# Kernel optimization log

Hardware: AMD Instinct MI355X
Metric: run time of the kernel (lower is better)

Reference implementation:

```python
import jax, jax.numpy as jnp
import numpy as np

B, T, C, H = 4, 2048, 1024, 16
D = C // H  # head dim = 64

def setup_inputs() -> dict:
    key = jax.random.key(0)
    k1, k2, k3 = jax.random.split(key, 3)
    x = jax.random.normal(k1, (B, T, C), dtype=jnp.float32)
    # torch Linear weight [out,in]; store transposed for x @ W
    W_attn = jax.random.normal(k2, (C, 3 * C), dtype=jnp.float32) * (1.0 / np.sqrt(C))
    W_proj = jax.random.normal(k3, (C, C), dtype=jnp.float32) * (1.0 / np.sqrt(C))
    return {"x": x, "W_attn": W_attn, "W_proj": W_proj}

def reference(x, W_attn, W_proj):
    qkv = x @ W_attn                          # [B,T,3C]
    q, k, v = jnp.split(qkv, 3, axis=-1)
    # [B,T,C] -> [B,H,T,D]
    def heads(t):
        return t.reshape(B, T, H, D).transpose(0, 2, 1, 3)
    q, k, v = heads(q), heads(k), heads(v)
    att = jnp.einsum('bhqd,bhkd->bhqk', q, k) * (1.0 / np.sqrt(D))  # [B,H,T,T]
    causal = jnp.tril(jnp.ones((T, T), dtype=bool))
    att = jnp.where(causal[None, None, :, :], att, -jnp.inf)
    att = jax.nn.softmax(att, axis=-1)
    y = jnp.einsum('bhqk,bhkd->bhqd', att, v)  # [B,H,T,D]
    y = y.transpose(0, 2, 1, 3).reshape(B, T, C)
    return y @ W_proj
```

## Files before the change

### kernel.cpp

```cpp
#include <hip/hip_runtime.h>
#include <hip/hip_bf16.h>

#define BB 4
#define TT 2048
#define CC 1024
#define HH 16
#define DD 64
#define MM (BB*TT)

typedef unsigned short u16;
typedef __bf16 bf16x8 __attribute__((ext_vector_type(8)));
typedef __bf16 bf16x4v __attribute__((ext_vector_type(4)));
typedef u16 u16x8 __attribute__((ext_vector_type(8)));
typedef u16 u16x4 __attribute__((ext_vector_type(4)));
typedef float f32x4 __attribute__((ext_vector_type(4)));

__device__ __forceinline__ u16 f2bf(float f) {
  union { float f; unsigned u; } v; v.f = f;
  unsigned u = v.u;
  return (u16)((u + 0x7fffu + ((u >> 16) & 1u)) >> 16);
}
__device__ __forceinline__ float bf2f(u16 s) {
  union { unsigned u; float f; } v; v.u = ((unsigned)s) << 16; return v.f;
}
__device__ __forceinline__ bf16x8 ld_bf16x8(const u16* p) {
  return *reinterpret_cast<const bf16x8*>(p);
}
__device__ __forceinline__ f32x4 zero4() {
  f32x4 z; z[0] = 0.f; z[1] = 0.f; z[2] = 0.f; z[3] = 0.f; return z;
}

__device__ __forceinline__ void gld_lds16(const u16* g, u16* l) {
  __builtin_amdgcn_global_load_lds(
      (const __attribute__((address_space(1))) void*)g,
      (__attribute__((address_space(3))) void*)l, 16, 0, 0);
}
__device__ __forceinline__ void wait_vm0() { __builtin_amdgcn_s_waitcnt(0x0F70); }
__device__ __forceinline__ void wait_vm2() { __builtin_amdgcn_s_waitcnt(0x0F72); }
__device__ __forceinline__ void wait_vm4() { __builtin_amdgcn_s_waitcnt(0x0F74); }

__device__ __forceinline__ float lane_pull(float x, int srclane) {
  int r = __builtin_amdgcn_ds_bpermute(srclane << 2, __builtin_bit_cast(int, x));
  return __builtin_bit_cast(float, r);
}

#define NC4B ((MM * CC / 4) / 256)
__global__ void k_prep(const float* __restrict__ x, u16* __restrict__ xb,
                       const float* __restrict__ Wa, u16* __restrict__ Wab,
                       const float* __restrict__ Wp, u16* __restrict__ Wpb) {
  __shared__ float tile[32][33];
  const int bx = blockIdx.x;
  if (bx < NC4B) {
    int i = bx * 256 + threadIdx.x;
    const float4 v = reinterpret_cast<const float4*>(x)[i];
    u16x4 r; r.x = f2bf(v.x); r.y = f2bf(v.y); r.z = f2bf(v.z); r.w = f2bf(v.w);
    reinterpret_cast<u16x4*>(xb)[i] = r;
    return;
  }
  const float* W; u16* Wt; int K, N, b2;
  if (bx < NC4B + 3072) { W = Wa; Wt = Wab; K = CC; N = 3 * CC; b2 = bx - NC4B; }
  else                  { W = Wp; Wt = Wpb; K = CC; N = CC;     b2 = bx - NC4B - 3072; }
  const int nblk = N / 32;
  const int nb = (b2 % nblk) * 32, kb = (b2 / nblk) * 32;
  const int tx = threadIdx.x & 31, ty = threadIdx.x >> 5;
  #pragma unroll
  for (int i = ty; i < 32; i += 8)
    tile[i][tx] = W[(size_t)(kb + i) * N + nb + tx];
  __syncthreads();
  #pragma unroll
  for (int i = ty; i < 32; i += 8)
    Wt[(size_t)(nb + i) * K + kb + tx] = f2bf(tile[tx][i]);
}

template<int EPI>
__global__ __launch_bounds__(256, 3)
void k_gemm_bt(const u16* __restrict__ A, const u16* __restrict__ Bt,
               float* __restrict__ outF, u16* __restrict__ qb, u16* __restrict__ kb,
               u16* __restrict__ vt, int N, int K)
{
  __shared__ u16 As[128 * 64];
  __shared__ u16 Bs[128 * 64];
  const int tid  = threadIdx.x;
  const int lane = tid & 63, w = tid >> 6;
  const int l16  = lane & 15, quad = lane >> 4;
  const int wr = w >> 1, wc = w & 1;
  const int m0 = blockIdx.y * 128, n0 = blockIdx.x * 128;
  const int lr8 = lane >> 3, lc8 = lane & 7;

  f32x4 acc[4][4];
  #pragma unroll
  for (int i = 0; i < 4; ++i)
    #pragma unroll
    for (int j = 0; j < 4; ++j) acc[i][j] = zero4();

  for (int k0 = 0; k0 < K; k0 += 64) {
    __syncthreads();
    #pragma unroll
    for (int p = 0; p < 4; ++p) {
      const int row = w * 32 + p * 8 + lr8;
      const int cs  = lc8 ^ (row & 7);
      gld_lds16(A  + (size_t)(m0 + row) * K + k0 + cs * 8, &As[(w * 32 + p * 8) * 64]);
      gld_lds16(Bt + (size_t)(n0 + row) * K + k0 + cs * 8, &Bs[(w * 32 + p * 8) * 64]);
    }
    wait_vm0();
    __syncthreads();
    #pragma unroll
    for (int s = 0; s < 2; ++s) {
      bf16x8 af[4], bfr[4];
      #pragma unroll
      for (int i = 0; i < 4; ++i) {
        int mrow = wr * 64 + i * 16 + l16;
        af[i]  = ld_bf16x8(&As[mrow * 64 + ((s * 4 + quad) ^ (l16 & 7)) * 8]);
        int nrow = wc * 64 + i * 16 + l16;
        bfr[i] = ld_bf16x8(&Bs[nrow * 64 + ((s * 4 + quad) ^ (l16 & 7)) * 8]);
      }
      #pragma unroll
      for (int i = 0; i < 4; ++i)
        #pragma unroll
        for (int j = 0; j < 4; ++j)
          acc[i][j] = __builtin_amdgcn_mfma_f32_16x16x32_bf16(af[i], bfr[j], acc[i][j], 0, 0, 0);
    }
  }

  #pragma unroll
  for (int i = 0; i < 4; ++i) {
    #pragma unroll
    for (int j = 0; j < 4; ++j) {
      const int n = n0 + wc * 64 + j * 16 + l16;
      const int mb = m0 + wr * 64 + i * 16 + quad * 4;
      if (EPI == 0) {
        #pragma unroll
        for (int r = 0; r < 4; ++r)
          outF[(size_t)(mb + r) * N + n] = acc[i][j][r];
      } else {
        const int b = mb >> 11, tb = mb & 2047;
        if (n < CC) {
          const int h = n >> 6, d = n & 63;
          #pragma unroll
          for (int r = 0; r < 4; ++r)
            qb[(((size_t)(b * HH + h) * TT + tb + r) << 6) + d] = f2bf(acc[i][j][r]);
        } else if (n < 2 * CC) {
          const int n2 = n - CC; const int h = n2 >> 6, d = n2 & 63;
          #pragma unroll
          for (int r = 0; r < 4; ++r)
            kb[(((size_t)(b * HH + h) * TT + tb + r) << 6) + d] = f2bf(acc[i][j][r]);
        } else {
          const int n2 = n - 2 * CC; const int h = n2 >> 6, d = n2 & 63;
          u16x4 cv;
          #pragma unroll
          for (int r = 0; r < 4; ++r) cv[r] = f2bf(acc[i][j][r]);
          *reinterpret_cast<u16x4*>(
              vt + ((size_t)(b * HH + h) * DD + d) * TT + tb) = cv;
        }
      }
    }
  }
}

__device__ __forceinline__ void stage_half256(const u16* __restrict__ G, u16* lbase,
                                              int grow0, int kk, int lr8, int lc8) {
  const int cs = (lc8 ^ lr8) << 3;
  gld_lds16(G + (size_t)(grow0 + lr8) * CC + kk + cs, lbase);
  gld_lds16(G + (size_t)(grow0 + 8 + lr8) * CC + kk + cs, lbase + 8 * 64);
}

__global__ __launch_bounds__(512, 2)
void k_gemm256(const u16* __restrict__ A, const u16* __restrict__ Bt,
               u16* __restrict__ qb, u16* __restrict__ kbuf, u16* __restrict__ vt)
{
  __shared__ u16 As[2][256 * 64];
  __shared__ u16 Bs[2][256 * 64];
  const int tid  = threadIdx.x;
  const int lane = tid & 63, w = tid >> 6;
  const int l16  = lane & 15, quad = lane >> 4;
  const int lr8  = lane >> 3, lc8 = lane & 7;
  const int wm = w >> 2, wn = w & 3;

  const int lin = blockIdx.x;
  const int nl  = (lin & 7) * 48 + (lin >> 3);
  const int mt  = nl / 12, nt_ = nl % 12;
  const int m0 = mt * 256, n0 = nt_ * 256;

  f32x4 acc[4][4][2];
  #pragma unroll
  for (int q = 0; q < 4; ++q)
    #pragma unroll
    for (int i = 0; i < 4; ++i)
      #pragma unroll
      for (int j = 0; j < 2; ++j) acc[q][i][j] = zero4();

  stage_half256(A,  &As[0][(0 * 128 + w * 16) * 64], m0 +       w * 16, 0, lr8, lc8);
  stage_half256(Bt, &Bs[0][(0 * 128 + w * 16) * 64], n0 +       w * 16, 0, lr8, lc8);
  stage_half256(Bt, &Bs[0][(1 * 128 + w * 16) * 64], n0 + 128 + w * 16, 0, lr8, lc8);
  stage_half256(A,  &As[0][(1 * 128 + w * 16) * 64], m0 + 128 + w * 16, 0, lr8, lc8);
  wait_vm4();
  __builtin_amdgcn_s_barrier();

  for (int t = 0; t < 16; ++t) {
    const int bb = t & 1;
    const bool notlast = (t < 15);
    const int kk = (t + 1) << 6;
    #pragma unroll
    for (int q = 0; q < 4; ++q) {
      const int qm = (q >> 1);
      const int qn = (q == 1 || q == 2);
      bf16x8 af[2][4], bfr[2][2];
      #pragma unroll
      for (int s = 0; s < 2; ++s) {
        const int cs = ((s * 4 + quad) ^ (l16 & 7)) << 3;
        #pragma unroll
        for (int i = 0; i < 4; ++i)
          af[s][i] = ld_bf16x8(&As[bb][(qm * 128 + wm * 64 + i * 16 + l16) * 64 + cs]);
        #pragma unroll
        for (int j = 0; j < 2; ++j)
          bfr[s][j] = ld_bf16x8(&Bs[bb][(qn * 128 + wn * 32 + j * 16 + l16) * 64 + cs]);
      }
      if (notlast) {
        if (q == 0)
          stage_half256(A,  &As[bb ^ 1][(0 * 128 + w * 16) * 64], m0 +       w * 16, kk, lr8, lc8);
        else if (q == 1)
          stage_half256(Bt, &Bs[bb ^ 1][(0 * 128 + w * 16) * 64], n0 +       w * 16, kk, lr8, lc8);
        else if (q == 2)
          stage_half256(Bt, &Bs[bb ^ 1][(1 * 128 + w * 16) * 64], n0 + 128 + w * 16, kk, lr8, lc8);
        else
          stage_half256(A,  &As[bb ^ 1][(1 * 128 + w * 16) * 64], m0 + 128 + w * 16, kk, lr8, lc8);
      }
      __builtin_amdgcn_s_setprio(1);
      #pragma unroll
      for (int s = 0; s < 2; ++s)
        #pragma unroll
        for (int i = 0; i < 4; ++i)
          #pragma unroll
          for (int j = 0; j < 2; ++j)
            acc[q][i][j] = __builtin_amdgcn_mfma_f32_16x16x32_bf16(
                af[s][i], bfr[s][j], acc[q][i][j], 0, 0, 0);
      __builtin_amdgcn_s_setprio(0);
      if (notlast)       wait_vm4();
      else if (q == 0)   wait_vm2();
      else if (q == 1)   wait_vm0();
      __builtin_amdgcn_s_barrier();
    }
  }

  #pragma unroll
  for (int q = 0; q < 4; ++q) {
    const int qm = (q >> 1);
    const int qn = (q == 1 || q == 2);
    #pragma unroll
    for (int i = 0; i < 4; ++i) {
      #pragma unroll
      for (int j = 0; j < 2; ++j) {
        const int n  = n0 + qn * 128 + wn * 32 + j * 16 + l16;
        const int mb = m0 + qm * 128 + wm * 64 + i * 16 + quad * 4;
        const int b = mb >> 11, tb = mb & 2047;
        if (n < CC) {
          const int h = n >> 6, d = n & 63;
          #pragma unroll
          for (int r = 0; r < 4; ++r)
            qb[(((size_t)(b * HH + h) * TT + tb + r) << 6) + d] = f2bf(acc[q][i][j][r]);
        } else if (n < 2 * CC) {
          const int n2 = n - CC; const int h = n2 >> 6, d = n2 & 63;
          #pragma unroll
          for (int r = 0; r < 4; ++r)
            kbuf[(((size_t)(b * HH + h) * TT + tb + r) << 6) + d] = f2bf(acc[q][i][j][r]);
        } else {
          const int n2 = n - 2 * CC; const int h = n2 >> 6, d = n2 & 63;
          u16x4 cv;
          #pragma unroll
          for (int r = 0; r < 4; ++r) cv[r] = f2bf(acc[q][i][j][r]);
          *reinterpret_cast<u16x4*>(
              vt + ((size_t)(b * HH + h) * DD + d) * TT + tb) = cv;
        }
      }
    }
  }
}

__global__ __launch_bounds__(256, 3)
void k_attn(const u16* __restrict__ qb, const u16* __restrict__ kb,
            const u16* __restrict__ vt, u16* __restrict__ y)
{
  __shared__ u16 Ks[128 * 64];
  __shared__ u16 Vs[64 * 128];
  __shared__ u16 QP[8 * 1024];
  const int tid  = threadIdx.x;
  const int lane = tid & 63, w = tid >> 6;
  const int l16  = lane & 15, quad = lane >> 4;
  const int lr8 = lane >> 3, lc8 = lane & 7;

  const int bx = blockIdx.x;
  const int qt = 15 - (bx >> 6);
  const int bh = bx & 63;
  const int h  = bh & 15, b = bh >> 4;

  const u16* qptr = qb + ((size_t)bh * TT + qt * 128) * DD;
  const u16* kptr = kb + (size_t)bh * TT * DD;
  const u16* vptr = vt + (size_t)bh * DD * TT;

  const float qscale = 0.125f * 1.44269504088896340736f;
  #pragma unroll
  for (int p = 0; p < 4; ++p) {
    const int r = w * 32 + p * 8 + lr8;
    u16x8 v = *reinterpret_cast<const u16x8*>(qptr + (size_t)r * DD + lc8 * 8);
    u16x8 o;
    #pragma unroll
    for (int e = 0; e < 8; ++e) o[e] = f2bf(bf2f(v[e]) * qscale);
    *reinterpret_cast<u16x8*>(&Ks[r * 64 + (lc8 ^ lr8) * 8]) = o;
  }
  __syncthreads();
  bf16x8 qf0[2], qf1[2];
  #pragma unroll
  for (int s = 0; s < 2; ++s) {
    qf0[s] = ld_bf16x8(&Ks[(w * 16 + l16) * 64 + ((s * 4 + quad) ^ (l16 & 7)) * 8]);
    qf1[s] = ld_bf16x8(&Ks[(64 + w * 16 + l16) * 64 + ((s * 4 + quad) ^ (l16 & 7)) * 8]);
  }

  float rsum0 = 0.f, rsum1 = 0.f;
  f32x4 O0[4], O1[4];
  #pragma unroll
  for (int j = 0; j < 4; ++j) { O0[j] = zero4(); O1[j] = zero4(); }

  const int nkt = qt + 1;
  for (int kt = 0; kt < nkt; ++kt) {
    __syncthreads();
    {
      const u16* kt0 = kptr + (size_t)kt * 128 * DD;
      #pragma unroll
      for (int p = 0; p < 4; ++p) {
        const int row = w * 32 + p * 8 + lr8;
        const int cs  = lc8 ^ lr8;
        gld_lds16(kt0 + (size_t)row * DD + cs * 8, &Ks[(w * 32 + p * 8) * 64]);
      }
      #pragma unroll
      for (int p = 0; p < 4; ++p) {
        const int d  = w * 16 + p * 4 + (lane >> 4);
        const int cs = (lane & 15) ^ (d & 7);
        gld_lds16(vptr + (size_t)d * TT + kt * 128 + cs * 8,
                  &Vs[(w * 16 + p * 4) * 128]);
      }
    }
    wait_vm0();
    __syncthreads();

    #pragma unroll
    for (int h2 = 0; h2 < 2; ++h2) {
      const int  last = (kt == qt);
      const bool g0on = !(last && h2 == 1);
      f32x4 St0[4], St1[4];
      #pragma unroll
      for (int j = 0; j < 4; ++j) { St0[j] = zero4(); St1[j] = zero4(); }
      #pragma unroll
      for (int s = 0; s < 2; ++s) {
        bf16x8 kfr[4];
        #pragma unroll
        for (int j = 0; j < 4; ++j)
          kfr[j] = ld_bf16x8(&Ks[(h2 * 64 + j * 16 + l16) * 64 +
                                 ((s * 4 + quad) ^ (l16 & 7)) * 8]);
        if (g0on) {
          #pragma unroll
          for (int j = 0; j < 4; ++j)
            St0[j] = __builtin_amdgcn_mfma_f32_16x16x32_bf16(kfr[j], qf0[s], St0[j], 0, 0, 0);
        }
        #pragma unroll
        for (int j = 0; j < 4; ++j)
          St1[j] = __builtin_amdgcn_mfma_f32_16x16x32_bf16(kfr[j], qf1[s], St1[j], 0, 0, 0);
      }
      if (last) {
        const int qg = w * 16 + l16;
        if (h2 == 0) {
          #pragma unroll
          for (int j = 0; j < 4; ++j)
            #pragma unroll
            for (int r = 0; r < 4; ++r)
              if (j * 16 + quad * 4 + r > qg) St0[j][r] = -__builtin_inff();
        } else {
          #pragma unroll
          for (int j = 0; j < 4; ++j)
            #pragma unroll
            for (int r = 0; r < 4; ++r)
              if (j * 16 + quad * 4 + r > qg) St1[j][r] = -__builtin_inff();
        }
      }

      if (g0on) {
        #pragma unroll
        for (int j = 0; j < 4; ++j)
          #pragma unroll
          for (int r = 0; r < 4; ++r) {
            float p = __builtin_amdgcn_exp2f(St0[j][r]);
            St0[j][r] = p; rsum0 += p;
          }
        #pragma unroll
        for (int j = 0; j < 4; ++j) {
          union { bf16x4v bv; u16x4 u; } cv;
          cv.bv[0] = (__bf16)St0[j][0]; cv.bv[1] = (__bf16)St0[j][1];
          cv.bv[2] = (__bf16)St0[j][2]; cv.bv[3] = (__bf16)St0[j][3];
          const int c = j * 2 + (quad >> 1);
          const int off = (w * 2 + 0) * 1024 + l16 * 64 +
                          ((c ^ (l16 & 7)) << 3) + ((quad & 1) << 2);
          *reinterpret_cast<u16x4*>(&QP[off]) = cv.u;
        }
      }
      #pragma unroll
      for (int j = 0; j < 4; ++j)
        #pragma unroll
        for (int r = 0; r < 4; ++r) {
          float p = __builtin_amdgcn_exp2f(St1[j][r]);
          St1[j][r] = p; rsum1 += p;
        }
      #pragma unroll
      for (int j = 0; j < 4; ++j) {
        union { bf16x4v bv; u16x4 u; } cv;
        cv.bv[0] = (__bf16)St1[j][0]; cv.bv[1] = (__bf16)St1[j][1];
        cv.bv[2] = (__bf16)St1[j][2]; cv.bv[3] = (__bf16)St1[j][3];
        const int c = j * 2 + (quad >> 1);
        const int off = (w * 2 + 1) * 1024 + l16 * 64 +
                        ((c ^ (l16 & 7)) << 3) + ((quad & 1) << 2);
        *reinterpret_cast<u16x4*>(&QP[off]) = cv.u;
      }

      #pragma unroll
      for (int s = 0; s < 2; ++s) {
        bf16x8 pf0, pf1;
        if (g0on)
          pf0 = ld_bf16x8(&QP[(w * 2 + 0) * 1024 + l16 * 64 +
                              ((s * 4 + quad) ^ (l16 & 7)) * 8]);
        pf1 = ld_bf16x8(&QP[(w * 2 + 1) * 1024 + l16 * 64 +
                            ((s * 4 + quad) ^ (l16 & 7)) * 8]);
        #pragma unroll
        for (int j = 0; j < 4; ++j) {
          bf16x8 vf = ld_bf16x8(&Vs[(j * 16 + l16) * 128 +
                                    ((h2 * 8 + s * 4 + quad) ^ (l16 & 7)) * 8]);
          if (g0on)
            O0[j] = __builtin_amdgcn_mfma_f32_16x16x32_bf16(pf0, vf, O0[j], 0, 0, 0);
          O1[j] = __builtin_amdgcn_mfma_f32_16x16x32_bf16(pf1, vf, O1[j], 0, 0, 0);
        }
      }
    }
  }

  #pragma unroll
  for (int g = 0; g < 2; ++g) {
    float rs = (g == 0) ? rsum0 : rsum1;
    rs += __shfl_xor(rs, 16);
    rs += __shfl_xor(rs, 32);
    const float linv = 1.0f / rs;
    f32x4 lv;
    #pragma unroll
    for (int r = 0; r < 4; ++r) lv[r] = lane_pull(linv, quad * 4 + r);
    #pragma unroll
    for (int j = 0; j < 4; ++j) {
      f32x4 o = (g == 0) ? O0[j] : O1[j];
      o *= lv;
      #pragma unroll
      for (int r = 0; r < 4; ++r) {
        int t  = qt * 128 + g * 64 + w * 16 + quad * 4 + r;
        int ch = h * 64 + j * 16 + l16;
        y[(size_t)(b * TT + t) * CC + ch] = f2bf(o[r]);
      }
    }
  }
}

extern "C" void kernel_launch(void* const* d_in, const int* in_sizes, int n_in,
                              void* d_out, int out_size, void* d_ws, size_t ws_size,
                              hipStream_t stream) {
  const float* x  = (const float*)d_in[0];
  const float* Wa = (const float*)d_in[1];
  const float* Wp = (const float*)d_in[2];
  float* out = (float*)d_out;

  u16* ws   = (u16*)d_ws;
  u16* xb   = ws;
  u16* Wab  = xb   + (size_t)MM * CC;
  u16* Wpb  = Wab  + (size_t)3 * CC * CC;
  u16* qbuf = Wpb  + (size_t)CC * CC;
  u16* kbuf = qbuf + (size_t)MM * CC;
  u16* vtb  = kbuf + (size_t)MM * CC;
  u16* yb   = vtb  + (size_t)MM * CC;

  k_prep<<<NC4B + 3072 + 1024, 256, 0, stream>>>(x, xb, Wa, Wab, Wp, Wpb);
  k_gemm256<<<384, 512, 0, stream>>>(xb, Wab, qbuf, kbuf, vtb);
  k_attn<<<64 * 16, 256, 0, stream>>>(qbuf, kbuf, vtb, yb);
  k_gemm_bt<0><<<dim3(CC / 128, MM / 128), 256, 0, stream>>>(
      yb, Wpb, out, nullptr, nullptr, nullptr, CC, CC);
}
```

Baseline: 245.9 us.

## Restructure QKV GEMM mainloop into HipKittens-style 8-wave ping-pong quadrant schedule

```diff
diff --git a/kernel.cpp b/kernel.cpp
--- a/kernel.cpp
+++ b/kernel.cpp
@@ -36,8 +36,7 @@
       (__attribute__((address_space(3))) void*)l, 16, 0, 0);
 }
 __device__ __forceinline__ void wait_vm0() { __builtin_amdgcn_s_waitcnt(0x0F70); }
-__device__ __forceinline__ void wait_vm2() { __builtin_amdgcn_s_waitcnt(0x0F72); }
-__device__ __forceinline__ void wait_vm4() { __builtin_amdgcn_s_waitcnt(0x0F74); }
+__device__ __forceinline__ void wait_vm6() { __builtin_amdgcn_s_waitcnt(0x0F76); }
 
 __device__ __forceinline__ float lane_pull(float x, int srclane) {
   int r = __builtin_amdgcn_ds_bpermute(srclane << 2, __builtin_bit_cast(int, x));
@@ -168,8 +167,8 @@
 void k_gemm256(const u16* __restrict__ A, const u16* __restrict__ Bt,
                u16* __restrict__ qb, u16* __restrict__ kbuf, u16* __restrict__ vt)
 {
-  __shared__ u16 As[2][256 * 64];
-  __shared__ u16 Bs[2][256 * 64];
+  __shared__ u16 As[2][2][128 * 64];
+  __shared__ u16 Bs[2][2][128 * 64];
   const int tid  = threadIdx.x;
   const int lane = tid & 63, w = tid >> 6;
   const int l16  = lane & 15, quad = lane >> 4;
@@ -181,95 +180,157 @@
   const int mt  = nl / 12, nt_ = nl % 12;
   const int m0 = mt * 256, n0 = nt_ * 256;
 
-  f32x4 acc[4][4][2];
-  #pragma unroll
-  for (int q = 0; q < 4; ++q)
-    #pragma unroll
-    for (int i = 0; i < 4; ++i)
-      #pragma unroll
-      for (int j = 0; j < 2; ++j) acc[q][i][j] = zero4();
-
-  stage_half256(A,  &As[0][(0 * 128 + w * 16) * 64], m0 +       w * 16, 0, lr8, lc8);
-  stage_half256(Bt, &Bs[0][(0 * 128 + w * 16) * 64], n0 +       w * 16, 0, lr8, lc8);
-  stage_half256(Bt, &Bs[0][(1 * 128 + w * 16) * 64], n0 + 128 + w * 16, 0, lr8, lc8);
-  stage_half256(A,  &As[0][(1 * 128 + w * 16) * 64], m0 + 128 + w * 16, 0, lr8, lc8);
-  wait_vm4();
+  f32x4 acc[2][2][4][2];
+  #pragma unroll
+  for (int qm = 0; qm < 2; ++qm)
+    #pragma unroll
+    for (int qn = 0; qn < 2; ++qn)
+      #pragma unroll
+      for (int i = 0; i < 4; ++i)
+        #pragma unroll
+        for (int j = 0; j < 2; ++j) acc[qm][qn][i][j] = zero4();
+
+  stage_half256(A,  &As[0][0][(w * 16) * 64], m0 +       w * 16,  0, lr8, lc8);
+  stage_half256(Bt, &Bs[0][0][(w * 16) * 64], n0 +       w * 16,  0, lr8, lc8);
+  stage_half256(Bt, &Bs[0][1][(w * 16) * 64], n0 + 128 + w * 16,  0, lr8, lc8);
+  stage_half256(A,  &As[0][1][(w * 16) * 64], m0 + 128 + w * 16,  0, lr8, lc8);
+  stage_half256(A,  &As[1][0][(w * 16) * 64], m0 +       w * 16, 64, lr8, lc8);
+  stage_half256(Bt, &Bs[1][0][(w * 16) * 64], n0 +       w * 16, 64, lr8, lc8);
+  stage_half256(Bt, &Bs[1][1][(w * 16) * 64], n0 + 128 + w * 16, 64, lr8, lc8);
+  wait_vm6();
   __builtin_amdgcn_s_barrier();
 
   for (int t = 0; t < 16; ++t) {
-    const int bb = t & 1;
-    const bool notlast = (t < 15);
-    const int kk = (t + 1) << 6;
-    #pragma unroll
-    for (int q = 0; q < 4; ++q) {
-      const int qm = (q >> 1);
-      const int qn = (q == 1 || q == 2);
-      bf16x8 af[2][4], bfr[2][2];
-      #pragma unroll
-      for (int s = 0; s < 2; ++s) {
-        const int cs = ((s * 4 + quad) ^ (l16 & 7)) << 3;
-        #pragma unroll
-        for (int i = 0; i < 4; ++i)
-          af[s][i] = ld_bf16x8(&As[bb][(qm * 128 + wm * 64 + i * 16 + l16) * 64 + cs]);
+    const int buf = t & 1;
+    const u16* A0p = &As[buf][0][0];
+    const u16* A1p = &As[buf][1][0];
+    const u16* B0p = &Bs[buf][0][0];
+    const u16* B1p = &Bs[buf][1][0];
+    bf16x8 afr[2][4], b0r[2][2], b1r[2][2];
+
+    #pragma unroll
+    for (int s = 0; s < 2; ++s) {
+      const int cs = ((s * 4 + quad) ^ (l16 & 7)) << 3;
+      #pragma unroll
+      for (int i = 0; i < 4; ++i)
+        afr[s][i] = ld_bf16x8(&A0p[(wm * 64 + i * 16 + l16) * 64 + cs]);
+      #pragma unroll
+      for (int j = 0; j < 2; ++j)
+        b0r[s][j] = ld_bf16x8(&B0p[(wn * 32 + j * 16 + l16) * 64 + cs]);
+    }
+    if (t < 15)
+      stage_half256(A, &As[buf ^ 1][1][(w * 16) * 64], m0 + 128 + w * 16,
+                    (t + 1) << 6, lr8, lc8);
+    __builtin_amdgcn_s_barrier();
+    asm volatile("s_waitcnt lgkmcnt(0)" ::: "memory");
+    __builtin_amdgcn_s_setprio(1);
+    #pragma unroll
+    for (int s = 0; s < 2; ++s)
+      #pragma unroll
+      for (int i = 0; i < 4; ++i)
         #pragma unroll
         for (int j = 0; j < 2; ++j)
-          bfr[s][j] = ld_bf16x8(&Bs[bb][(qn * 128 + wn * 32 + j * 16 + l16) * 64 + cs]);
-      }
-      if (notlast) {
-        if (q == 0)
-          stage_half256(A,  &As[bb ^ 1][(0 * 128 + w * 16) * 64], m0 +       w * 16, kk, lr8, lc8);
-        else if (q == 1)
-          stage_half256(Bt, &Bs[bb ^ 1][(0 * 128 + w * 16) * 64], n0 +       w * 16, kk, lr8, lc8);
-        else if (q == 2)
-          stage_half256(Bt, &Bs[bb ^ 1][(1 * 128 + w * 16) * 64], n0 + 128 + w * 16, kk, lr8, lc8);
-        else
-          stage_half256(A,  &As[bb ^ 1][(1 * 128 + w * 16) * 64], m0 + 128 + w * 16, kk, lr8, lc8);
-      }
-      __builtin_amdgcn_s_setprio(1);
-      #pragma unroll
-      for (int s = 0; s < 2; ++s)
-        #pragma unroll
-        for (int i = 0; i < 4; ++i)
-          #pragma unroll
-          for (int j = 0; j < 2; ++j)
-            acc[q][i][j] = __builtin_amdgcn_mfma_f32_16x16x32_bf16(
-                af[s][i], bfr[s][j], acc[q][i][j], 0, 0, 0);
-      __builtin_amdgcn_s_setprio(0);
-      if (notlast)       wait_vm4();
-      else if (q == 0)   wait_vm2();
-      else if (q == 1)   wait_vm0();
-      __builtin_amdgcn_s_barrier();
-    }
-  }
-
-  #pragma unroll
-  for (int q = 0; q < 4; ++q) {
-    const int qm = (q >> 1);
-    const int qn = (q == 1 || q == 2);
-    #pragma unroll
-    for (int i = 0; i < 4; ++i) {
-      #pragma unroll
-      for (int j = 0; j < 2; ++j) {
-        const int n  = n0 + qn * 128 + wn * 32 + j * 16 + l16;
-        const int mb = m0 + qm * 128 + wm * 64 + i * 16 + quad * 4;
-        const int b = mb >> 11, tb = mb & 2047;
-        if (n < CC) {
-          const int h = n >> 6, d = n & 63;
-          #pragma unroll
-          for (int r = 0; r < 4; ++r)
-            qb[(((size_t)(b * HH + h) * TT + tb + r) << 6) + d] = f2bf(acc[q][i][j][r]);
-        } else if (n < 2 * CC) {
-          const int n2 = n - CC; const int h = n2 >> 6, d = n2 & 63;
-          #pragma unroll
-          for (int r = 0; r < 4; ++r)
-            kbuf[(((size_t)(b * HH + h) * TT + tb + r) << 6) + d] = f2bf(acc[q][i][j][r]);
-        } else {
-          const int n2 = n - 2 * CC; const int h = n2 >> 6, d = n2 & 63;
-          u16x4 cv;
-          #pragma unroll
-          for (int r = 0; r < 4; ++r) cv[r] = f2bf(acc[q][i][j][r]);
-          *reinterpret_cast<u16x4*>(
-              vt + ((size_t)(b * HH + h) * DD + d) * TT + tb) = cv;
+          acc[0][0][i][j] = __builtin_amdgcn_mfma_f32_16x16x32_bf16(
+              afr[s][i], b0r[s][j], acc[0][0][i][j], 0, 0, 0);
+    __builtin_amdgcn_s_setprio(0);
+    __builtin_amdgcn_s_barrier();
+
+    #pragma unroll
+    for (int s = 0; s < 2; ++s) {
+      const int cs = ((s * 4 + quad) ^ (l16 & 7)) << 3;
+      #pragma unroll
+      for (int j = 0; j < 2; ++j)
+        b1r[s][j] = ld_bf16x8(&B1p[(wn * 32 + j * 16 + l16) * 64 + cs]);
+    }
+    if (t < 14)
+      stage_half256(A, &As[buf][0][(w * 16) * 64], m0 + w * 16,
+                    (t + 2) << 6, lr8, lc8);
+    __builtin_amdgcn_s_barrier();
+    asm volatile("s_waitcnt lgkmcnt(0)" ::: "memory");
+    __builtin_amdgcn_s_setprio(1);
+    #pragma unroll
+    for (int s = 0; s < 2; ++s)
+      #pragma unroll
+      for (int i = 0; i < 4; ++i)
+        #pragma unroll
+        for (int j = 0; j < 2; ++j)
+          acc[0][1][i][j] = __builtin_amdgcn_mfma_f32_16x16x32_bf16(
+              afr[s][i], b1r[s][j], acc[0][1][i][j], 0, 0, 0);
+    __builtin_amdgcn_s_setprio(0);
+    __builtin_amdgcn_s_barrier();
+
+    #pragma unroll
+    for (int s = 0; s < 2; ++s) {
+      const int cs = ((s * 4 + quad) ^ (l16 & 7)) << 3;
+      #pragma unroll
+      for (int i = 0; i < 4; ++i)
+        afr[s][i] = ld_bf16x8(&A1p[(wm * 64 + i * 16 + l16) * 64 + cs]);
+    }
+    if (t < 14)
+      stage_half256(Bt, &Bs[buf][0][(w * 16) * 64], n0 + w * 16,
+                    (t + 2) << 6, lr8, lc8);
+    __builtin_amdgcn_s_barrier();
+    asm volatile("s_waitcnt lgkmcnt(0)" ::: "memory");
+    __builtin_amdgcn_s_setprio(1);
+    #pragma unroll
+    for (int s = 0; s < 2; ++s)
+      #pragma unroll
+      for (int i = 0; i < 4; ++i)
+        #pragma unroll
+        for (int j = 0; j < 2; ++j)
+          acc[1][1][i][j] = __builtin_amdgcn_mfma_f32_16x16x32_bf16(
+              afr[s][i], b1r[s][j], acc[1][1][i][j], 0, 0, 0);
+    __builtin_amdgcn_s_setprio(0);
+    __builtin_amdgcn_s_barrier();
+
+    if (t < 14)
+      stage_half256(Bt, &Bs[buf][1][(w * 16) * 64], n0 + 128 + w * 16,
+                    (t + 2) << 6, lr8, lc8);
+    __builtin_amdgcn_s_barrier();
+    asm volatile("s_waitcnt lgkmcnt(0)" ::: "memory");
+    __builtin_amdgcn_s_setprio(1);
+    #pragma unroll
+    for (int s = 0; s < 2; ++s)
+      #pragma unroll
+      for (int i = 0; i < 4; ++i)
+        #pragma unroll
+        for (int j = 0; j < 2; ++j)
+          acc[1][0][i][j] = __builtin_amdgcn_mfma_f32_16x16x32_bf16(
+              afr[s][i], b0r[s][j], acc[1][0][i][j], 0, 0, 0);
+    __builtin_amdgcn_s_setprio(0);
+    if (t < 14) wait_vm6(); else wait_vm0();
+    __builtin_amdgcn_s_barrier();
+  }
+
+  #pragma unroll
+  for (int qm = 0; qm < 2; ++qm) {
+    #pragma unroll
+    for (int qn = 0; qn < 2; ++qn) {
+      #pragma unroll
+      for (int i = 0; i < 4; ++i) {
+        #pragma unroll
+        for (int j = 0; j < 2; ++j) {
+          const int n  = n0 + qn * 128 + wn * 32 + j * 16 + l16;
+          const int mb = m0 + qm * 128 + wm * 64 + i * 16 + quad * 4;
+          const int b = mb >> 11, tb = mb & 2047;
+          if (n < CC) {
+            const int h = n >> 6, d = n & 63;
+            #pragma unroll
+            for (int r = 0; r < 4; ++r)
+              qb[(((size_t)(b * HH + h) * TT + tb + r) << 6) + d] = f2bf(acc[qm][qn][i][j][r]);
+          } else if (n < 2 * CC) {
+            const int n2 = n - CC; const int h = n2 >> 6, d = n2 & 63;
+            #pragma unroll
+            for (int r = 0; r < 4; ++r)
+              kbuf[(((size_t)(b * HH + h) * TT + tb + r) << 6) + d] = f2bf(acc[qm][qn][i][j][r]);
+          } else {
+            const int n2 = n - 2 * CC; const int h = n2 >> 6, d = n2 & 63;
+            u16x4 cv;
+            #pragma unroll
+            for (int r = 0; r < 4; ++r) cv[r] = f2bf(acc[qm][qn][i][j][r]);
+            *reinterpret_cast<u16x4*>(
+                vt + ((size_t)(b * HH + h) * DD + d) * TT + tb) = cv;
+          }
         }
       }
     }
```

New measurement: 236.3 us. 3.9% less time.
